# Kernel optimization log

Hardware: AMD Instinct MI355X
Metric: run time of the kernel (lower is better)

## Reference

```python
import jax, jax.numpy as jnp
import numpy as np
import math

IN_F = 1024
OUT_F = 1024
B = 16
L = 4096  # img_size (number of positions)


def setup_inputs() -> dict:
    key = jax.random.key(0)
    k1, k2, k3 = jax.random.split(key, 3)
    Efou = jax.random.normal(k1, (B, L, IN_F), dtype=jnp.float32)
    y = jax.random.normal(k2, (B, IN_F), dtype=jnp.float32)
    weight = jax.random.normal(k3, (1, OUT_F, IN_F, 1), dtype=jnp.float32)
    return {"Efou": Efou, "y": y, "weight": weight}


def reference(Efou, y, weight):
    b, img_size, in_f = Efou.shape
    out_f = weight.shape[1]
    scale = 1.0 / math.sqrt(in_f)
    # per-sample modulated weights: [B, out, in]
    w = scale * weight[:, :, :, 0] * y[:, None, :]
    # demodulation norm over the input-feature axis
    dnorm = jax.lax.rsqrt(jnp.sum(w * w, axis=2, keepdims=True) + 1e-8)  # [B, out, 1]
    w = w * dnorm
    # faithful to torch: Efou.reshape(1, B*in, L) is a raw row-major reshape
    E = Efou.reshape(b, in_f, img_size)  # [B, in, L] (same bytes as original)
    x = jnp.einsum('boi,bil->bol', w, E)  # grouped conv1d, kernel size 1
    # faithful to torch: x.view(B, L, out) is a raw reshape of [B, out, L]
    return x.reshape(b, img_size, out_f)
```

## Files before the change

kernel.cpp:

```cpp
#include <hip/hip_runtime.h>
#include <hip/hip_bf16.h>
#include <cstdint>
#include <cstddef>

typedef __bf16 bf16x8 __attribute__((ext_vector_type(8)));
typedef __bf16 bf16x4 __attribute__((ext_vector_type(4)));
typedef float f32x4 __attribute__((ext_vector_type(4)));

#define BATCH 16
#define MDIM 1024
#define NDIM 4096
#define KDIM 1024
#define BM 256
#define BN 256
#define BK 64
#define NKT (KDIM / BK)

__device__ __forceinline__ void gload_lds16(const void* g, void* l) {
  __builtin_amdgcn_global_load_lds(
      (const __attribute__((address_space(1))) void*)g,
      (__attribute__((address_space(3))) void*)l, 16, 0, 0);
}

#define BAR() __builtin_amdgcn_s_barrier()
#define SB() __builtin_amdgcn_sched_barrier(0)
#define FENCE() asm volatile("" ::: "memory")
#define LGKM0()                                        \
  do {                                                 \
    asm volatile("s_waitcnt lgkmcnt(0)" ::: "memory"); \
    SB();                                              \
  } while (0)
#define VMC32()                                        \
  do {                                                 \
    asm volatile("s_waitcnt vmcnt(32)" ::: "memory");  \
    SB();                                              \
  } while (0)
#define VMC0()                                         \
  do {                                                 \
    asm volatile("s_waitcnt vmcnt(0)" ::: "memory");   \
    SB();                                              \
  } while (0)

__global__ __launch_bounds__(256) void modw_kernel(
    const float* __restrict__ weight, const float* __restrict__ y,
    __bf16* __restrict__ wm) {
  const int blk = blockIdx.x;
  const int b = blk & 15;
  const int o = blk >> 4;
  const int t = threadIdx.x;
  const float4 w4 = reinterpret_cast<const float4*>(weight + (size_t)o * KDIM)[t];
  const float4 y4 = reinterpret_cast<const float4*>(y + (size_t)b * KDIM)[t];
  const float p0 = w4.x * y4.x, p1 = w4.y * y4.y;
  const float p2 = w4.z * y4.z, p3 = w4.w * y4.w;
  float s = p0 * p0 + p1 * p1 + p2 * p2 + p3 * p3;
#pragma unroll
  for (int off = 32; off >= 1; off >>= 1) s += __shfl_xor(s, off, 64);
  __shared__ float ps[4];
  if ((t & 63) == 0) ps[t >> 6] = s;
  __syncthreads();
  const float tot = ps[0] + ps[1] + ps[2] + ps[3];
  const float scale = 0.03125f;
  const float dn = scale * rsqrtf(scale * scale * tot + 1e-8f);
  bf16x4 v;
  v[0] = (__bf16)(p0 * dn);
  v[1] = (__bf16)(p1 * dn);
  v[2] = (__bf16)(p2 * dn);
  v[3] = (__bf16)(p3 * dn);
  *reinterpret_cast<bf16x4*>(wm + ((size_t)b * MDIM + o) * KDIM + t * 4) = v;
}

__global__ __launch_bounds__(512, 2) void gemm_kernel(
    const __bf16* __restrict__ Wm, const float* __restrict__ E,
    float* __restrict__ out) {
  const int orig = blockIdx.x;
  const int wg = (orig & 7) * 128 + (orig >> 3);
  const int mt = wg & 3;
  const int nt = (wg >> 2) & 15;
  const int b = wg >> 6;
  const int m0 = mt * BM, n0 = nt * BN;

  __shared__ __align__(16) char smem[131072];
  char* const A0_ = smem;
  char* const A1_ = smem + 32768;
  char* const B0_ = smem + 65536;
  char* const B1_ = smem + 98304;

  const int tid = threadIdx.x;
  const int lane = tid & 63;
  const int wid = tid >> 6;
  const int wr = wid >> 2;
  const int wc = wid & 3;
  const int ml = lane & 15;
  const int kg = lane >> 4;

  const int arow = tid >> 3;
  const int aswz = ((tid & 7) ^ (arow & 7)) * 8;
  const __bf16* Ag = Wm + ((size_t)(b * MDIM + m0 + arow)) * KDIM + aswz;
  const int aldsOff = tid * 16;

  const int bn1 = tid & 63;
  const int bkg = tid >> 6;
  typedef const __attribute__((address_space(1))) float gfloat;
  gfloat* Eg = (gfloat*)(E + (size_t)b * KDIM * NDIM +
                         (size_t)(bkg * 8) * NDIM + n0 + bn1);
  int bwr[4];
#pragma unroll
  for (int c = 0; c < 4; ++c) {
    const int n = bn1 + 64 * c;
    bwr[c] = n * 128 + ((bkg * 16) ^ ((n & 7) << 4));
  }

  const int colA = (kg * 16) ^ ((ml & 7) << 4);
  const int arB = (wr * 128 + ml) * 128;
  const int brB = (wc * 64 + ml) * 128;

  f32x4 acc[8][4];
#pragma unroll
  for (int i = 0; i < 8; ++i)
#pragma unroll
    for (int j = 0; j < 4; ++j) acc[i][j] = (f32x4){0.f, 0.f, 0.f, 0.f};

  auto stageA = [&](char* Ab, int kt) {
#pragma unroll
    for (int r = 0; r < 4; ++r)
      gload_lds16(Ag + (size_t)(64 * r) * KDIM + kt * BK,
                  Ab + aldsOff + r * 8192);
  };
  auto loadB = [&](float (&brr)[4][8], int kt) {
#pragma unroll
    for (int c = 0; c < 4; ++c)
#pragma unroll
      for (int j = 0; j < 8; ++j)
        brr[c][j] = Eg[(size_t)(kt * BK + j) * NDIM + 64 * c];
  };
  auto writeB = [&](char* Bb, float (&brr)[4][8]) {
#pragma unroll
    for (int c = 0; c < 4; ++c) {
      bf16x8 v;
#pragma unroll
      for (int j = 0; j < 8; ++j) v[j] = (__bf16)brr[c][j];
      *reinterpret_cast<bf16x8*>(Bb + bwr[c]) = v;
    }
  };

  float br[4][8];

  {
    float brT[4][8];
    stageA(A0_, 0);
    FENCE();
    SB();
    loadB(brT, 0);
    writeB(B0_, brT);
    loadB(br, 1);
    LGKM0();
    BAR();
  }

  char* Ac = A0_;
  char* Ao = A1_;
  char* Bc = B0_;
  char* Bo = B1_;

#pragma unroll 1
  for (int t = 0; t < NKT; ++t) {
    if (t + 1 < NKT) {
      writeB(Bo, br);
      stageA(Ao, t + 1);
      FENCE();
      SB();
    }
    if (t + 2 < NKT) loadB(br, t + 2);

#pragma unroll
    for (int kk = 0; kk < 2; ++kk) {
      const int kx = colA ^ (kk * 64);
      bf16x8 af[4], bf[4];
#pragma unroll
      for (int nf = 0; nf < 4; ++nf)
        bf[nf] = *reinterpret_cast<const bf16x8*>(Bc + brB + nf * 2048 + kx);
#pragma unroll
      for (int i = 0; i < 4; ++i)
        af[i] = *reinterpret_cast<const bf16x8*>(Ac + arB + i * 2048 + kx);
      __builtin_amdgcn_s_setprio(1);
#pragma unroll
      for (int i = 0; i < 4; ++i)
#pragma unroll
        for (int nf = 0; nf < 4; ++nf)
          acc[i][nf] = __builtin_amdgcn_mfma_f32_16x16x32_bf16(
              af[i], bf[nf], acc[i][nf], 0, 0, 0);
      __builtin_amdgcn_s_setprio(0);
#pragma unroll
      for (int i = 0; i < 4; ++i)
        af[i] = *reinterpret_cast<const bf16x8*>(Ac + arB + (4 + i) * 2048 + kx);
      __builtin_amdgcn_s_setprio(1);
#pragma unroll
      for (int i = 0; i < 4; ++i)
#pragma unroll
        for (int nf = 0; nf < 4; ++nf)
          acc[4 + i][nf] = __builtin_amdgcn_mfma_f32_16x16x32_bf16(
              af[i], bf[nf], acc[4 + i][nf], 0, 0, 0);
      __builtin_amdgcn_s_setprio(0);
    }

    if (t + 2 < NKT) {
      VMC32();
    } else {
      VMC0();
    }
    LGKM0();
    BAR();

    char* ta = Ac; Ac = Ao; Ao = ta;
    char* tb = Bc; Bc = Bo; Bo = tb;
  }

  float* ob = out + ((size_t)(b * MDIM + m0 + wr * 128 + kg * 4)) * NDIM +
              n0 + wc * 64 + ml;
#pragma unroll
  for (int mf = 0; mf < 8; ++mf)
#pragma unroll
    for (int nf = 0; nf < 4; ++nf) {
      const f32x4 a = acc[mf][nf];
      float* p = ob + (size_t)mf * 16 * NDIM + nf * 16;
#pragma unroll
      for (int q = 0; q < 4; ++q) p[(size_t)q * NDIM] = a[q];
    }
}

extern "C" void kernel_launch(void* const* d_in, const int* in_sizes, int n_in,
                              void* d_out, int out_size, void* d_ws,
                              size_t ws_size, hipStream_t stream) {
  (void)in_sizes;
  (void)n_in;
  (void)out_size;
  (void)ws_size;
  const float* Efou = (const float*)d_in[0];
  const float* y = (const float*)d_in[1];
  const float* weight = (const float*)d_in[2];
  float* outp = (float*)d_out;
  __bf16* wm = (__bf16*)d_ws;

  modw_kernel<<<dim3(BATCH * MDIM), dim3(256), 0, stream>>>(weight, y, wm);
  gemm_kernel<<<dim3(BATCH * (MDIM / BM) * (NDIM / BN)), dim3(512), 0,
                stream>>>(wm, Efou, outp);
}
```

Before: 213.3 us.

## Pre-transpose E to bf16 K-major and stage both GEMM operands via LDS DMA

Adds a separate kernel that converts the fp32 E activations to a bf16 [B,N,K] K-major layout in workspace. The GEMM can then load both operands with global_load_lds into swizzled LDS instead of doing per-thread fp32 register loads, conversions and LDS writes. The main loop is restructured into four barrier-separated quarter phases that interleave the next tile's prefetch with the MFMA work. The cost is an extra pass over E (read 256MB, write 128MB) plus an extra launch, with a fallback to the old GEMM path when the workspace is too small.

```diff
diff --git a/kernel.cpp b/kernel.cpp
--- a/kernel.cpp
+++ b/kernel.cpp
@@ -69,7 +69,181 @@
   *reinterpret_cast<bf16x4*>(wm + ((size_t)b * MDIM + o) * KDIM + t * 4) = v;
 }
 
+__global__ __launch_bounds__(256) void transE_kernel(
+    const float* __restrict__ E, __bf16* __restrict__ Eb) {
+  const int blk = blockIdx.x;
+  const int ntile = blk & 63;
+  const int kt = (blk >> 6) & 15;
+  const int b = blk >> 10;
+  const int t = threadIdx.x;
+  __shared__ float tile[64][65];
+  const int tn = (t & 15) * 4;
+  const int tk = t >> 4;
+  const float* src =
+      E + ((size_t)(b * KDIM + kt * 64)) * NDIM + ntile * 64;
+#pragma unroll
+  for (int r = 0; r < 4; ++r) {
+    const int k = tk + 16 * r;
+    const float4 v =
+        *reinterpret_cast<const float4*>(src + (size_t)k * NDIM + tn);
+    tile[k][tn + 0] = v.x;
+    tile[k][tn + 1] = v.y;
+    tile[k][tn + 2] = v.z;
+    tile[k][tn + 3] = v.w;
+  }
+  __syncthreads();
+  const int wk = (t & 15) * 4;
+  __bf16* dst = Eb + ((size_t)(b * NDIM + ntile * 64)) * KDIM +
+                (size_t)kt * 64 + wk;
+#pragma unroll
+  for (int r = 0; r < 4; ++r) {
+    const int n = (t >> 4) + 16 * r;
+    bf16x4 v;
+    v[0] = (__bf16)tile[wk + 0][n];
+    v[1] = (__bf16)tile[wk + 1][n];
+    v[2] = (__bf16)tile[wk + 2][n];
+    v[3] = (__bf16)tile[wk + 3][n];
+    *reinterpret_cast<bf16x4*>(dst + (size_t)n * KDIM) = v;
+  }
+}
+
 __global__ __launch_bounds__(512, 2) void gemm_kernel(
+    const __bf16* __restrict__ Wm, const __bf16* __restrict__ Ebt,
+    float* __restrict__ out) {
+  const int orig = blockIdx.x;
+  const int wg = (orig & 7) * 128 + (orig >> 3);
+  const int mt = wg & 3;
+  const int nt = (wg >> 2) & 15;
+  const int b = wg >> 6;
+  const int m0 = mt * BM, n0 = nt * BN;
+
+  __shared__ __align__(16) char smem[131072];
+  char* const A0_ = smem;
+  char* const A1_ = smem + 32768;
+  char* const B0_ = smem + 65536;
+  char* const B1_ = smem + 98304;
+
+  const int tid = threadIdx.x;
+  const int lane = tid & 63;
+  const int wid = tid >> 6;
+  const int wr = wid >> 2;
+  const int wc = wid & 3;
+  const int ml = lane & 15;
+  const int kg = lane >> 4;
+
+  const int srow = tid >> 3;
+  const int sswz = ((tid & 7) ^ (srow & 7)) * 8;
+  const __bf16* Ag = Wm + ((size_t)(b * MDIM + m0 + srow)) * KDIM + sswz;
+  const __bf16* Bg = Ebt + ((size_t)(b * NDIM + n0 + srow)) * KDIM + sswz;
+  const int sldsOff = tid * 16;
+
+  const int colA = (kg * 16) ^ ((ml & 7) << 4);
+  const int arB = (wr * 128 + ml) * 128;
+  const int brB = (wc * 64 + ml) * 128;
+
+  f32x4 acc[8][4];
+#pragma unroll
+  for (int i = 0; i < 8; ++i)
+#pragma unroll
+    for (int j = 0; j < 4; ++j) acc[i][j] = (f32x4){0.f, 0.f, 0.f, 0.f};
+
+  auto stageA = [&](char* Ab, int kt) {
+#pragma unroll
+    for (int r = 0; r < 4; ++r)
+      gload_lds16(Ag + (size_t)(64 * r) * KDIM + kt * BK,
+                  Ab + sldsOff + r * 8192);
+  };
+  auto stageB = [&](char* Bb, int kt) {
+#pragma unroll
+    for (int r = 0; r < 4; ++r)
+      gload_lds16(Bg + (size_t)(64 * r) * KDIM + kt * BK,
+                  Bb + sldsOff + r * 8192);
+  };
+
+#define RD_B(Bc, KKv)                                          \
+  do {                                                         \
+    _Pragma("unroll") for (int nf = 0; nf < 4; ++nf)           \
+        bf[nf] = *reinterpret_cast<const bf16x8*>(             \
+            (Bc) + brB + nf * 2048 + (colA ^ ((KKv)*64)));     \
+  } while (0)
+#define RD_A(Ac, QMv, KKv)                                         \
+  do {                                                             \
+    _Pragma("unroll") for (int i = 0; i < 4; ++i)                  \
+        af[i] = *reinterpret_cast<const bf16x8*>(                  \
+            (Ac) + arB + ((QMv)*4 + i) * 2048 + (colA ^ ((KKv)*64))); \
+  } while (0)
+#define MFMA16(QMv)                                                      \
+  do {                                                                   \
+    __builtin_amdgcn_s_setprio(1);                                       \
+    _Pragma("unroll") for (int i = 0; i < 4; ++i)                        \
+        _Pragma("unroll") for (int nf = 0; nf < 4; ++nf)                 \
+            acc[(QMv)*4 + i][nf] = __builtin_amdgcn_mfma_f32_16x16x32_bf16( \
+                af[i], bf[nf], acc[(QMv)*4 + i][nf], 0, 0, 0);           \
+    __builtin_amdgcn_s_setprio(0);                                       \
+  } while (0)
+
+  stageA(A0_, 0);
+  stageB(B0_, 0);
+  VMC0();
+  BAR();
+
+  char* Ac = A0_;
+  char* Ao = A1_;
+  char* Bc = B0_;
+  char* Bo = B1_;
+
+#pragma unroll 1
+  for (int t = 0; t < NKT; ++t) {
+    bf16x8 af[4], bf[4];
+    const bool pf = (t + 1 < NKT);
+
+    RD_B(Bc, 0);
+    RD_A(Ac, 0, 0);
+    if (pf) stageA(Ao, t + 1);
+    BAR();
+    LGKM0();
+    MFMA16(0);
+    BAR();
+    RD_A(Ac, 1, 0);
+    if (pf) stageB(Bo, t + 1);
+    BAR();
+    LGKM0();
+    MFMA16(1);
+    BAR();
+    RD_B(Bc, 1);
+    RD_A(Ac, 0, 1);
+    BAR();
+    LGKM0();
+    MFMA16(0);
+    BAR();
+    RD_A(Ac, 1, 1);
+    BAR();
+    LGKM0();
+    MFMA16(1);
+    VMC0();
+    BAR();
+
+    char* ta = Ac; Ac = Ao; Ao = ta;
+    char* tb = Bc; Bc = Bo; Bo = tb;
+  }
+#undef RD_B
+#undef RD_A
+#undef MFMA16
+
+  float* ob = out + ((size_t)(b * MDIM + m0 + wr * 128 + kg * 4)) * NDIM +
+              n0 + wc * 64 + ml;
+#pragma unroll
+  for (int mf = 0; mf < 8; ++mf)
+#pragma unroll
+    for (int nf = 0; nf < 4; ++nf) {
+      const f32x4 a = acc[mf][nf];
+      float* p = ob + (size_t)mf * 16 * NDIM + nf * 16;
+#pragma unroll
+      for (int q = 0; q < 4; ++q) p[(size_t)q * NDIM] = a[q];
+    }
+}
+
+__global__ __launch_bounds__(512, 2) void gemm_fb_kernel(
     const __bf16* __restrict__ Wm, const float* __restrict__ E,
     float* __restrict__ out) {
   const int orig = blockIdx.x;
@@ -149,7 +323,6 @@
     float brT[4][8];
     stageA(A0_, 0);
     FENCE();
-    SB();
     loadB(brT, 0);
     writeB(B0_, brT);
     loadB(br, 1);
@@ -168,7 +341,6 @@
       writeB(Bo, br);
       stageA(Ao, t + 1);
       FENCE();
-      SB();
     }
     if (t + 2 < NKT) loadB(br, t + 2);
 
@@ -234,14 +406,24 @@
   (void)in_sizes;
   (void)n_in;
   (void)out_size;
-  (void)ws_size;
   const float* Efou = (const float*)d_in[0];
   const float* y = (const float*)d_in[1];
   const float* weight = (const float*)d_in[2];
   float* outp = (float*)d_out;
   __bf16* wm = (__bf16*)d_ws;
+  const size_t wm_bytes = (size_t)BATCH * MDIM * KDIM * 2;
+  const size_t eb_bytes = (size_t)BATCH * NDIM * KDIM * 2;
 
   modw_kernel<<<dim3(BATCH * MDIM), dim3(256), 0, stream>>>(weight, y, wm);
-  gemm_kernel<<<dim3(BATCH * (MDIM / BM) * (NDIM / BN)), dim3(512), 0,
-                stream>>>(wm, Efou, outp);
-}
+
+  if (ws_size >= wm_bytes + eb_bytes) {
+    __bf16* Eb = (__bf16*)((char*)d_ws + wm_bytes);
+    transE_kernel<<<dim3(BATCH * (KDIM / 64) * (NDIM / 64)), dim3(256), 0,
+                    stream>>>(Efou, Eb);
+    gemm_kernel<<<dim3(BATCH * (MDIM / BM) * (NDIM / BN)), dim3(512), 0,
+                  stream>>>(wm, Eb, outp);
+  } else {
+    gemm_fb_kernel<<<dim3(BATCH * (MDIM / BM) * (NDIM / BN)), dim3(512), 0,
+                     stream>>>(wm, Efou, outp);
+  }
+}
```

New measurement: 273.4 us. +28.2%, slower.

## Software-pipeline LDS fragment reads with MFMA and prefetch next tile across barrier

Applied to the files above, without the earlier changes.

Restructures the main K loop so LDS fragment reads for the next MFMA group are issued while the current group computes. Global loads, B-tile writes and A staging are interleaved between MFMA groups, and the first fragments of the next k-tile are read before the last MFMA group of the current tile. The aim is to hide LDS latency and the barrier stall behind matrix math. It adds extra fragment registers (af0/af1/bf0/bf1), which raises register pressure at two workgroups per CU, and it depends on correct wait and barrier ordering.

```diff
diff --git a/kernel.cpp b/kernel.cpp
--- a/kernel.cpp
+++ b/kernel.cpp
@@ -142,19 +142,44 @@
       *reinterpret_cast<bf16x8*>(Bb + bwr[c]) = v;
     }
   };
+  auto rdA = [&](bf16x8 (&d)[4], const char* Ab, int qm, int kk) {
+#pragma unroll
+    for (int i = 0; i < 4; ++i)
+      d[i] = *reinterpret_cast<const bf16x8*>(Ab + arB + (qm * 4 + i) * 2048 +
+                                              (colA ^ (kk * 64)));
+  };
+  auto rdB = [&](bf16x8 (&d)[4], const char* Bb, int kk) {
+#pragma unroll
+    for (int nf = 0; nf < 4; ++nf)
+      d[nf] = *reinterpret_cast<const bf16x8*>(Bb + brB + nf * 2048 +
+                                               (colA ^ (kk * 64)));
+  };
+  auto mfma16 = [&](bf16x8 (&a)[4], bf16x8 (&bv)[4], int qm) {
+    __builtin_amdgcn_s_setprio(1);
+#pragma unroll
+    for (int i = 0; i < 4; ++i)
+#pragma unroll
+      for (int nf = 0; nf < 4; ++nf)
+        acc[qm * 4 + i][nf] = __builtin_amdgcn_mfma_f32_16x16x32_bf16(
+            a[i], bv[nf], acc[qm * 4 + i][nf], 0, 0, 0);
+    __builtin_amdgcn_s_setprio(0);
+  };
 
   float br[4][8];
+  bf16x8 af0[4], af1[4];
+  bf16x8 bf0[4], bf1[4];
 
   {
     float brT[4][8];
     stageA(A0_, 0);
     FENCE();
-    SB();
     loadB(brT, 0);
     writeB(B0_, brT);
     loadB(br, 1);
     LGKM0();
     BAR();
+    rdA(af0, A0_, 0, 0);
+    rdB(bf0, B0_, 0);
   }
 
   char* Ac = A0_;
@@ -164,52 +189,35 @@
 
 #pragma unroll 1
   for (int t = 0; t < NKT; ++t) {
-    if (t + 1 < NKT) {
-      writeB(Bo, br);
-      stageA(Ao, t + 1);
-      FENCE();
-      SB();
-    }
-    if (t + 2 < NKT) loadB(br, t + 2);
-
-#pragma unroll
-    for (int kk = 0; kk < 2; ++kk) {
-      const int kx = colA ^ (kk * 64);
-      bf16x8 af[4], bf[4];
-#pragma unroll
-      for (int nf = 0; nf < 4; ++nf)
-        bf[nf] = *reinterpret_cast<const bf16x8*>(Bc + brB + nf * 2048 + kx);
-#pragma unroll
-      for (int i = 0; i < 4; ++i)
-        af[i] = *reinterpret_cast<const bf16x8*>(Ac + arB + i * 2048 + kx);
-      __builtin_amdgcn_s_setprio(1);
-#pragma unroll
-      for (int i = 0; i < 4; ++i)
-#pragma unroll
-        for (int nf = 0; nf < 4; ++nf)
-          acc[i][nf] = __builtin_amdgcn_mfma_f32_16x16x32_bf16(
-              af[i], bf[nf], acc[i][nf], 0, 0, 0);
-      __builtin_amdgcn_s_setprio(0);
-#pragma unroll
-      for (int i = 0; i < 4; ++i)
-        af[i] = *reinterpret_cast<const bf16x8*>(Ac + arB + (4 + i) * 2048 + kx);
-      __builtin_amdgcn_s_setprio(1);
-#pragma unroll
-      for (int i = 0; i < 4; ++i)
-#pragma unroll
-        for (int nf = 0; nf < 4; ++nf)
-          acc[4 + i][nf] = __builtin_amdgcn_mfma_f32_16x16x32_bf16(
-              af[i], bf[nf], acc[4 + i][nf], 0, 0, 0);
-      __builtin_amdgcn_s_setprio(0);
-    }
-
-    if (t + 2 < NKT) {
+    const bool pf1 = (t + 1 < NKT);
+    const bool pf2 = (t + 2 < NKT);
+
+    rdA(af1, Ac, 1, 0);
+    if (pf1) writeB(Bo, br);
+    mfma16(af0, bf0, 0);
+
+    rdB(bf1, Bc, 1);
+    rdA(af0, Ac, 0, 1);
+    if (pf1) stageA(Ao, t + 1);
+    FENCE();
+    if (pf2) loadB(br, t + 2);
+    mfma16(af1, bf0, 1);
+
+    rdA(af1, Ac, 1, 1);
+    mfma16(af0, bf1, 0);
+    LGKM0();
+    if (pf2) {
       VMC32();
     } else {
       VMC0();
     }
-    LGKM0();
     BAR();
+
+    if (pf1) {
+      rdA(af0, Ao, 0, 0);
+      rdB(bf0, Bo, 0);
+    }
+    mfma16(af1, bf1, 1);
 
     char* ta = Ac; Ac = Ao; Ao = ta;
     char* tb = Bc; Bc = Bo; Bo = tb;
```

Result: no change. 211.6 us (median of 3 runs) (-0.8%).
